# Kernel optimization log

Measured on AMD Instinct MI355X. Metric: run time of the kernel, lower is better.

Reference implementation:

```python
import jax, jax.numpy as jnp
import numpy as np


def setup_inputs() -> dict:
    key = jax.random.key(0)
    k1, k2 = jax.random.split(key)
    x = jax.random.normal(k1, (64, 32, 32, 128), dtype=jnp.float32)
    embeddings = jax.random.normal(k2, (128, 1024), dtype=jnp.float32)  # (embedding_dim, num_embeddings)
    return {"x": x, "embeddings": embeddings}


def reference(x, embeddings):
    d = embeddings.shape[0]
    flat = x.reshape(-1, d)  # [N, d]
    # squared L2 distances: ||f||^2 + ||e||^2 - 2 f.e
    similarity = flat @ embeddings  # [N, K]
    distances = (jnp.sum(flat * flat, axis=1, keepdims=True)
                 + jnp.sum(embeddings * embeddings, axis=0)
                 - 2.0 * similarity)
    idx = jnp.argmin(distances, axis=1)  # [N]
    # gather codes (equivalent to one_hot @ embeddings^T)
    quantized = embeddings.T[idx].reshape(x.shape)
    # straight-through estimator
    quantized = x + jax.lax.stop_gradient(quantized - x)
    return quantized
```

## Files before the change

### kernel.cpp

```cpp
#include <hip/hip_runtime.h>


#define NROWS 65536
#define DDIM 128
#define KCODES 1024
#define MARGIN1 0.004f

typedef __attribute__((ext_vector_type(8))) short short8;
typedef __attribute__((ext_vector_type(16))) float f32x16;

__device__ inline ushort f2bf(float f) {
    union { float f; unsigned u; } v; v.f = f;
    unsigned r = v.u + 0x7fffu + ((v.u >> 16) & 1u);
    return (ushort)(r >> 16);
}
__device__ inline float bf2f(ushort b) {
    union { unsigned u; float f; } v; v.u = ((unsigned)b) << 16;
    return v.f;
}

__device__ inline void gload_lds16(const uint4* g, uint4* lds) {
    __builtin_amdgcn_global_load_lds((const __attribute__((address_space(1))) void*)g,
                                     (__attribute__((address_space(3))) void*)lds,
                                     16, 0, 0);
}

__global__ void k_prep(const float* __restrict__ e, float* __restrict__ et,
                       float* __restrict__ nrm, double* __restrict__ nrm64,
                       uint4* __restrict__ epq) {
    const int gid = blockIdx.x * blockDim.x + threadIdx.x;

    {
        int d = gid >> 10, k = gid & 1023;
        et[k * DDIM + d] = e[gid];
    }

    if (gid < 32768) {
        int lane = gid & 63, c = (gid >> 6) & 7, h = (gid >> 9) & 1, nt = gid >> 10;
        int col = nt * 32 + (lane & 31);
        int kbase = c * 16 + ((lane >> 5) << 3);
        union { ushort u[8]; uint4 q; } pk;
        #pragma unroll
        for (int j = 0; j < 8; ++j) {
            float v = e[(kbase + j) * KCODES + col];
            ushort hb = f2bf(v);
            pk.u[j] = (h == 0) ? hb : f2bf(v - bf2f(hb));
        }
        epq[(size_t)nt * 1024 + h * 512 + c * 64 + lane] = pk.q;
    }

    if (gid >= 32768 && gid < 32768 + 8192) {
        int t2 = gid - 32768;
        int k = t2 >> 3, part = t2 & 7;
        double s = 0.0;
        #pragma unroll
        for (int j = 0; j < 16; ++j) {
            double v = (double)e[(part * 16 + j) * KCODES + k];
            s = fma(v, v, s);
        }
        #pragma unroll
        for (int m = 1; m < 8; m <<= 1) s += __shfl_xor(s, m);
        if (part == 0) { nrm64[k] = s; nrm[k] = (float)s; }
    }
}

__global__ __launch_bounds__(256, 2) void k_argmin32(const float* __restrict__ x,
                                                     const uint4* __restrict__ epq,
                                                     const float* __restrict__ nrm,
                                                     float* __restrict__ pb1,
                                                     float* __restrict__ pb2,
                                                     int* __restrict__ pbi) {
    __shared__ uint4 sbuf[2][1024];
    __shared__ float snrm[512];

    const int tid = threadIdx.x;
    const int lane = tid & 63;
    const int w = tid >> 6;
    const int kh = blockIdx.x & 1;
    const int rg = blockIdx.x >> 1;
    const int rt = rg * 4 + w;
    const int lrow = lane & 31;
    const int lgrp = lane >> 5;
    const int tbase = kh * 16;

    #pragma unroll
    for (int i = 0; i < 4; ++i)
        gload_lds16(epq + (size_t)tbase * 1024 + i * 256 + tid,
                    &sbuf[0][i * 256 + (w << 6)]);

    snrm[tid] = nrm[kh * 512 + tid];
    snrm[256 + tid] = nrm[kh * 512 + 256 + tid];

    const float* xr = x + (size_t)(rt * 32 + lrow) * DDIM + (lgrp << 3);
    short8 ah[8], al[8];
    #pragma unroll
    for (int c = 0; c < 8; ++c) {
        float4 u = *reinterpret_cast<const float4*>(xr + c * 16);
        float4 v = *reinterpret_cast<const float4*>(xr + c * 16 + 4);
        float fv[8] = {u.x, u.y, u.z, u.w, v.x, v.y, v.z, v.w};
        short8 hi, lo;
        #pragma unroll
        for (int j = 0; j < 8; ++j) {
            ushort hb = f2bf(fv[j]);
            hi[j] = (short)hb;
            lo[j] = (short)f2bf(fv[j] - bf2f(hb));
        }
        ah[c] = hi; al[c] = lo;
    }

    float b1[16], b2[16]; int bi[16];
    #pragma unroll
    for (int r = 0; r < 16; ++r) { b1[r] = 3.4e38f; b2[r] = 3.4e38f; bi[r] = 0; }

    __syncthreads();

    int cur = 0;
    for (int t = 0; t < 16; ++t) {
        if (t + 1 < 16) {
            #pragma unroll
            for (int i = 0; i < 4; ++i)
                gload_lds16(epq + (size_t)(tbase + t + 1) * 1024 + i * 256 + tid,
                            &sbuf[cur ^ 1][i * 256 + (w << 6)]);
        }
        const int lcode = t * 32 + lrow;
        const float nv = snrm[lcode];
        const int code = kh * 512 + lcode;

        f32x16 accA, accB;
        #pragma unroll
        for (int r = 0; r < 16; ++r) { accA[r] = 0.f; accB[r] = 0.f; }

        #pragma unroll
        for (int c = 0; c < 8; ++c) {
            union { uint4 q; short8 s; } bh, bl;
            bh.q = sbuf[cur][c * 64 + lane];
            bl.q = sbuf[cur][512 + c * 64 + lane];
            accA = __builtin_amdgcn_mfma_f32_32x32x16_bf16(ah[c], bh.s, accA, 0, 0, 0);
            accA = __builtin_amdgcn_mfma_f32_32x32x16_bf16(ah[c], bl.s, accA, 0, 0, 0);
            accB = __builtin_amdgcn_mfma_f32_32x32x16_bf16(al[c], bh.s, accB, 0, 0, 0);
        }

        #pragma unroll
        for (int r = 0; r < 16; ++r) {
            float s = fmaf(-2.f, accA[r] + accB[r], nv);
            b2[r] = fminf(fmaxf(s, b1[r]), b2[r]);
            bool lt = s < b1[r];
            b1[r] = lt ? s : b1[r];
            bi[r] = lt ? code : bi[r];
        }
        __syncthreads();
        cur ^= 1;
    }

    #pragma unroll
    for (int r = 0; r < 16; ++r) {
        #pragma unroll
        for (int m = 1; m < 32; m <<= 1) {
            float o1 = __shfl_xor(b1[r], m);
            float o2 = __shfl_xor(b2[r], m);
            int   oi = __shfl_xor(bi[r], m);
            bool take = (o1 < b1[r]) || (o1 == b1[r] && oi < bi[r]);
            float loser = take ? b1[r] : o1;
            b1[r] = take ? o1 : b1[r];
            bi[r] = take ? oi : bi[r];
            b2[r] = fminf(fminf(b2[r], o2), loser);
        }
    }

    if (lrow == 0) {
        #pragma unroll
        for (int r = 0; r < 16; ++r) {
            int rl = (r & 3) + 8 * (r >> 2) + 4 * lgrp;
            size_t o = (size_t)kh * NROWS + rt * 32 + rl;
            pb1[o] = b1[r]; pb2[o] = b2[r]; pbi[o] = bi[r];
        }
    }
}

__global__ void k_merge(const float* __restrict__ pb1, const float* __restrict__ pb2,
                        const int* __restrict__ pbi, int* __restrict__ idx,
                        int* __restrict__ wlc, int* __restrict__ wl) {
    int r = blockIdx.x * blockDim.x + threadIdx.x;
    float a1 = pb1[r], a2 = pb2[r];
    int   ai = pbi[r];
    float c1 = pb1[NROWS + r], c2 = pb2[NROWS + r];
    int   ci = pbi[NROWS + r];
    bool take = c1 < a1;
    float f1 = take ? c1 : a1;
    int   fi = take ? ci : ai;
    float loser = take ? a1 : c1;
    float f2 = fminf(fminf(a2, c2), loser);
    idx[r] = fi;
    if (f2 - f1 < MARGIN1) {
        int slot = atomicAdd(wlc, 1);
        wl[slot] = r;
    }
}

__global__ __launch_bounds__(256) void k_fix(const float* __restrict__ x,
                                             const float* __restrict__ e,
                                             const double* __restrict__ nrm64,
                                             const int* __restrict__ wlc,
                                             const int* __restrict__ wl,
                                             int* __restrict__ idx) {
    __shared__ float  xs[DDIM];
    __shared__ double w1[4]; __shared__ int wi[4];
    const int tid = threadIdx.x;
    const int lane = tid & 63;
    const int wv = tid >> 6;
    const int n = *wlc;

    for (int i = blockIdx.x; i < n; i += gridDim.x) {
        const int row = wl[i];
        if (tid < DDIM) xs[tid] = x[(size_t)row * DDIM + tid];
        __syncthreads();

        double dot[4] = {0.0, 0.0, 0.0, 0.0};
        for (int d0 = 0; d0 < DDIM; d0 += 8) {
            float ef[8][4];
            #pragma unroll
            for (int dd = 0; dd < 8; ++dd)
                #pragma unroll
                for (int kk = 0; kk < 4; ++kk)
                    ef[dd][kk] = e[(d0 + dd) * KCODES + tid + kk * 256];
            #pragma unroll
            for (int dd = 0; dd < 8; ++dd) {
                double xv = (double)xs[d0 + dd];
                #pragma unroll
                for (int kk = 0; kk < 4; ++kk)
                    dot[kk] = fma(xv, (double)ef[dd][kk], dot[kk]);
            }
        }

        double bb1 = 1e300; int bbi = 0;
        #pragma unroll
        for (int kk = 0; kk < 4; ++kk) {
            int k = tid + kk * 256;
            double sc = nrm64[k] - 2.0 * dot[kk];
            if (sc < bb1) { bb1 = sc; bbi = k; }
        }
        #pragma unroll
        for (int m = 1; m < 64; m <<= 1) {
            double o1 = __shfl_xor(bb1, m);
            int    oi = __shfl_xor(bbi, m);
            bool take = (o1 < bb1) || (o1 == bb1 && oi < bbi);
            bb1 = take ? o1 : bb1;
            bbi = take ? oi : bbi;
        }
        if (lane == 0) { w1[wv] = bb1; wi[wv] = bbi; }
        __syncthreads();
        if (tid == 0) {
            double f1 = w1[0]; int fi = wi[0];
            #pragma unroll
            for (int j = 1; j < 4; ++j) {
                bool take = (w1[j] < f1) || (w1[j] == f1 && wi[j] < fi);
                f1 = take ? w1[j] : f1;
                fi = take ? wi[j] : fi;
            }
            idx[row] = fi;
        }
        __syncthreads();
    }
}

__global__ void k_gather(const float* __restrict__ x, const float* __restrict__ et,
                         const int* __restrict__ idxp, float* __restrict__ out) {
    int gid = blockIdx.x * blockDim.x + threadIdx.x;
    int row = gid >> 5, d4 = gid & 31;
    float4 q = reinterpret_cast<const float4*>(et)[(size_t)idxp[row] * 32 + d4];
    float4 xv = reinterpret_cast<const float4*>(x)[gid];
    float4 o;
    o.x = xv.x + (q.x - xv.x);
    o.y = xv.y + (q.y - xv.y);
    o.z = xv.z + (q.z - xv.z);
    o.w = xv.w + (q.w - xv.w);
    reinterpret_cast<float4*>(out)[gid] = o;
}

extern "C" void kernel_launch(void* const* d_in, const int* in_sizes, int n_in,
                              void* d_out, int out_size, void* d_ws, size_t ws_size,
                              hipStream_t stream) {
    const float* x = (const float*)d_in[0];
    const float* e = (const float*)d_in[1];
    float* out = (float*)d_out;

    double* nrm64 = (double*)d_ws;
    float*  et    = (float*)d_ws + 2048;
    float*  nrm   = et + 131072;
    int*    idx   = (int*)(nrm + 1024);
    int*    wlc   = idx + NROWS;
    int*    wl    = wlc + 4;
    uint4*  epq   = (uint4*)(wl + NROWS);
    float*  pb1   = (float*)(epq + 32768);
    float*  pb2   = pb1 + 2 * NROWS;
    int*    pbi   = (int*)(pb2 + 2 * NROWS);

    hipMemsetAsync(wlc, 0, sizeof(int), stream);

    k_prep<<<512, 256, 0, stream>>>(e, et, nrm, nrm64, epq);
    k_argmin32<<<1024, 256, 0, stream>>>(x, epq, nrm, pb1, pb2, pbi);
    k_merge<<<NROWS / 256, 256, 0, stream>>>(pb1, pb2, pbi, idx, wlc, wl);
    k_fix<<<64, 256, 0, stream>>>(x, e, nrm64, wlc, wl, idx);
    k_gather<<<(NROWS * 32) / 256, 256, 0, stream>>>(x, et, idx, out);
}
```

Measured before the change: 108.6 us.

## Use single bf16 MFMA coarse argmin with packed-key tracking and rescan near-ties

The main argmin pass drops the hi/lo bf16 split, running one MFMA per chunk instead of three. It also drops LDS staging in favour of direct global loads, and tracks max-similarity keys with the tile index packed into the low mantissa bits. Rows whose top-two gap is below a wider margin go to a new rescan kernel that redoes the split-precision distance over all codes. Only rows still within the tight margin reach the fp64 fix pass. This trades much less MFMA work in the bulk pass for an extra kernel and a rescan cost that grows with how many rows fall inside the wide margin.

```diff
diff --git a/kernel.cpp b/kernel.cpp
--- a/kernel.cpp
+++ b/kernel.cpp
@@ -4,7 +4,8 @@
 #define NROWS 65536
 #define DDIM 128
 #define KCODES 1024
-#define MARGIN1 0.004f
+#define MARGIN1 0.6f
+#define MARGIN2 0.004f
 
 typedef __attribute__((ext_vector_type(8))) short short8;
 typedef __attribute__((ext_vector_type(16))) float f32x16;
@@ -17,12 +18,6 @@
 __device__ inline float bf2f(ushort b) {
     union { unsigned u; float f; } v; v.u = ((unsigned)b) << 16;
     return v.f;
-}
-
-__device__ inline void gload_lds16(const uint4* g, uint4* lds) {
-    __builtin_amdgcn_global_load_lds((const __attribute__((address_space(1))) void*)g,
-                                     (__attribute__((address_space(3))) void*)lds,
-                                     16, 0, 0);
 }
 
 __global__ void k_prep(const float* __restrict__ e, float* __restrict__ et,
@@ -70,109 +65,79 @@
                                                      float* __restrict__ pb1,
                                                      float* __restrict__ pb2,
                                                      int* __restrict__ pbi) {
-    __shared__ uint4 sbuf[2][1024];
-    __shared__ float snrm[512];
-
     const int tid = threadIdx.x;
     const int lane = tid & 63;
     const int w = tid >> 6;
     const int kh = blockIdx.x & 1;
-    const int rg = blockIdx.x >> 1;
-    const int rt = rg * 4 + w;
+    const int rt = (blockIdx.x >> 1) * 4 + w;
     const int lrow = lane & 31;
     const int lgrp = lane >> 5;
     const int tbase = kh * 16;
 
-    #pragma unroll
-    for (int i = 0; i < 4; ++i)
-        gload_lds16(epq + (size_t)tbase * 1024 + i * 256 + tid,
-                    &sbuf[0][i * 256 + (w << 6)]);
-
-    snrm[tid] = nrm[kh * 512 + tid];
-    snrm[256 + tid] = nrm[kh * 512 + 256 + tid];
-
     const float* xr = x + (size_t)(rt * 32 + lrow) * DDIM + (lgrp << 3);
-    short8 ah[8], al[8];
+    short8 ah[8];
     #pragma unroll
     for (int c = 0; c < 8; ++c) {
         float4 u = *reinterpret_cast<const float4*>(xr + c * 16);
         float4 v = *reinterpret_cast<const float4*>(xr + c * 16 + 4);
         float fv[8] = {u.x, u.y, u.z, u.w, v.x, v.y, v.z, v.w};
-        short8 hi, lo;
-        #pragma unroll
-        for (int j = 0; j < 8; ++j) {
-            ushort hb = f2bf(fv[j]);
-            hi[j] = (short)hb;
-            lo[j] = (short)f2bf(fv[j] - bf2f(hb));
-        }
-        ah[c] = hi; al[c] = lo;
-    }
-
-    float b1[16], b2[16]; int bi[16];
+        short8 hi;
+        #pragma unroll
+        for (int j = 0; j < 8; ++j) hi[j] = (short)f2bf(fv[j]);
+        ah[c] = hi;
+    }
+
+    float kb1[16], kb2[16];
     #pragma unroll
-    for (int r = 0; r < 16; ++r) { b1[r] = 3.4e38f; b2[r] = 3.4e38f; bi[r] = 0; }
-
-    __syncthreads();
-
-    int cur = 0;
+    for (int r = 0; r < 16; ++r) { kb1[r] = -3.4e38f; kb2[r] = -3.4e38f; }
+
     for (int t = 0; t < 16; ++t) {
-        if (t + 1 < 16) {
-            #pragma unroll
-            for (int i = 0; i < 4; ++i)
-                gload_lds16(epq + (size_t)(tbase + t + 1) * 1024 + i * 256 + tid,
-                            &sbuf[cur ^ 1][i * 256 + (w << 6)]);
-        }
-        const int lcode = t * 32 + lrow;
-        const float nv = snrm[lcode];
-        const int code = kh * 512 + lcode;
-
-        f32x16 accA, accB;
-        #pragma unroll
-        for (int r = 0; r < 16; ++r) { accA[r] = 0.f; accB[r] = 0.f; }
+        const int nt = tbase + t;
+        const float nv = nrm[nt * 32 + lrow];
+
+        f32x16 acc;
+        #pragma unroll
+        for (int r = 0; r < 16; ++r) acc[r] = 0.f;
 
         #pragma unroll
         for (int c = 0; c < 8; ++c) {
-            union { uint4 q; short8 s; } bh, bl;
-            bh.q = sbuf[cur][c * 64 + lane];
-            bl.q = sbuf[cur][512 + c * 64 + lane];
-            accA = __builtin_amdgcn_mfma_f32_32x32x16_bf16(ah[c], bh.s, accA, 0, 0, 0);
-            accA = __builtin_amdgcn_mfma_f32_32x32x16_bf16(ah[c], bl.s, accA, 0, 0, 0);
-            accB = __builtin_amdgcn_mfma_f32_32x32x16_bf16(al[c], bh.s, accB, 0, 0, 0);
+            union { uint4 q; short8 s; } b;
+            b.q = epq[(size_t)nt * 1024 + c * 64 + lane];
+            acc = __builtin_amdgcn_mfma_f32_32x32x16_bf16(ah[c], b.s, acc, 0, 0, 0);
         }
 
         #pragma unroll
         for (int r = 0; r < 16; ++r) {
-            float s = fmaf(-2.f, accA[r] + accB[r], nv);
-            b2[r] = fminf(fmaxf(s, b1[r]), b2[r]);
-            bool lt = s < b1[r];
-            b1[r] = lt ? s : b1[r];
-            bi[r] = lt ? code : bi[r];
-        }
-        __syncthreads();
-        cur ^= 1;
+            float m = fmaf(-0.5f, nv, acc[r]);
+            float key = __uint_as_float((__float_as_uint(m) & 0xFFFFFFF0u) | (unsigned)t);
+            kb2[r] = fmaxf(kb2[r], fminf(key, kb1[r]));
+            kb1[r] = fmaxf(kb1[r], key);
+        }
     }
 
     #pragma unroll
     for (int r = 0; r < 16; ++r) {
-        #pragma unroll
-        for (int m = 1; m < 32; m <<= 1) {
-            float o1 = __shfl_xor(b1[r], m);
-            float o2 = __shfl_xor(b2[r], m);
-            int   oi = __shfl_xor(bi[r], m);
-            bool take = (o1 < b1[r]) || (o1 == b1[r] && oi < bi[r]);
-            float loser = take ? b1[r] : o1;
-            b1[r] = take ? o1 : b1[r];
-            bi[r] = take ? oi : bi[r];
-            b2[r] = fminf(fminf(b2[r], o2), loser);
-        }
-    }
-
-    if (lrow == 0) {
-        #pragma unroll
-        for (int r = 0; r < 16; ++r) {
+        unsigned u1 = __float_as_uint(kb1[r]);
+        int code = (tbase + (int)(u1 & 15u)) * 32 + lrow;
+        float m1 = __uint_as_float(u1 & 0xFFFFFFF0u);
+        float m2 = __uint_as_float(__float_as_uint(kb2[r]) & 0xFFFFFFF0u);
+        #pragma unroll
+        for (int mm = 1; mm < 32; mm <<= 1) {
+            float o1 = __shfl_xor(m1, mm);
+            float o2 = __shfl_xor(m2, mm);
+            int   oc = __shfl_xor(code, mm);
+            bool take = (o1 > m1) || (o1 == m1 && oc < code);
+            float loser = take ? m1 : o1;
+            m1 = take ? o1 : m1;
+            code = take ? oc : code;
+            m2 = fmaxf(fmaxf(m2, o2), loser);
+        }
+        if (lrow == 0) {
             int rl = (r & 3) + 8 * (r >> 2) + 4 * lgrp;
             size_t o = (size_t)kh * NROWS + rt * 32 + rl;
-            pb1[o] = b1[r]; pb2[o] = b2[r]; pbi[o] = bi[r];
+            pb1[o] = -2.f * m1;
+            pb2[o] = -2.f * m2;
+            pbi[o] = code;
         }
     }
 }
@@ -197,6 +162,101 @@
     }
 }
 
+__global__ __launch_bounds__(256, 2) void k_rescan(const float* __restrict__ x,
+                                                   const uint4* __restrict__ epq,
+                                                   const float* __restrict__ nrm,
+                                                   const int* __restrict__ wlc,
+                                                   const int* __restrict__ wl,
+                                                   int* __restrict__ idx,
+                                                   int* __restrict__ wl2c,
+                                                   int* __restrict__ wl2) {
+    const int tid = threadIdx.x;
+    const int lane = tid & 63;
+    const int w = tid >> 6;
+    const int lrow = lane & 31;
+    const int lgrp = lane >> 5;
+    const int n = *wlc;
+    const int ntiles = (n + 31) >> 5;
+
+    for (int it = blockIdx.x * 4 + w; it < ntiles; it += gridDim.x * 4) {
+        int li = it * 32 + lrow;
+        int rowl = wl[li < n ? li : 0];
+
+        const float* xr = x + (size_t)rowl * DDIM + (lgrp << 3);
+        short8 ah[8], al[8];
+        #pragma unroll
+        for (int c = 0; c < 8; ++c) {
+            float4 u = *reinterpret_cast<const float4*>(xr + c * 16);
+            float4 v = *reinterpret_cast<const float4*>(xr + c * 16 + 4);
+            float fv[8] = {u.x, u.y, u.z, u.w, v.x, v.y, v.z, v.w};
+            short8 hi, lo;
+            #pragma unroll
+            for (int j = 0; j < 8; ++j) {
+                ushort hb = f2bf(fv[j]);
+                hi[j] = (short)hb;
+                lo[j] = (short)f2bf(fv[j] - bf2f(hb));
+            }
+            ah[c] = hi; al[c] = lo;
+        }
+
+        float b1[16], b2[16]; int bi[16];
+        #pragma unroll
+        for (int r = 0; r < 16; ++r) { b1[r] = 3.4e38f; b2[r] = 3.4e38f; bi[r] = 0; }
+
+        for (int t = 0; t < 32; ++t) {
+            const float nv = nrm[t * 32 + lrow];
+            const int code = t * 32 + lrow;
+            f32x16 accA, accB;
+            #pragma unroll
+            for (int r = 0; r < 16; ++r) { accA[r] = 0.f; accB[r] = 0.f; }
+            #pragma unroll
+            for (int c = 0; c < 8; ++c) {
+                union { uint4 q; short8 s; } bh, bl;
+                bh.q = epq[(size_t)t * 1024 + c * 64 + lane];
+                bl.q = epq[(size_t)t * 1024 + 512 + c * 64 + lane];
+                accA = __builtin_amdgcn_mfma_f32_32x32x16_bf16(ah[c], bh.s, accA, 0, 0, 0);
+                accA = __builtin_amdgcn_mfma_f32_32x32x16_bf16(ah[c], bl.s, accA, 0, 0, 0);
+                accB = __builtin_amdgcn_mfma_f32_32x32x16_bf16(al[c], bh.s, accB, 0, 0, 0);
+            }
+            #pragma unroll
+            for (int r = 0; r < 16; ++r) {
+                float s = fmaf(-2.f, accA[r] + accB[r], nv);
+                b2[r] = fminf(fmaxf(s, b1[r]), b2[r]);
+                bool lt = s < b1[r];
+                b1[r] = lt ? s : b1[r];
+                bi[r] = lt ? code : bi[r];
+            }
+        }
+
+        #pragma unroll
+        for (int r = 0; r < 16; ++r) {
+            #pragma unroll
+            for (int mm = 1; mm < 32; mm <<= 1) {
+                float o1 = __shfl_xor(b1[r], mm);
+                float o2 = __shfl_xor(b2[r], mm);
+                int   oi = __shfl_xor(bi[r], mm);
+                bool take = (o1 < b1[r]) || (o1 == b1[r] && oi < bi[r]);
+                float loser = take ? b1[r] : o1;
+                b1[r] = take ? o1 : b1[r];
+                bi[r] = take ? oi : bi[r];
+                b2[r] = fminf(fminf(b2[r], o2), loser);
+            }
+            if (lrow == 0) {
+                int rl = (r & 3) + 8 * (r >> 2) + 4 * lgrp;
+                int lj = it * 32 + rl;
+                if (lj < n) {
+                    int row = wl[lj];
+                    idx[row] = bi[r];
+                    if (b2[r] - b1[r] < MARGIN2) {
+                        int slot = atomicAdd(wl2c, 1);
+                        wl2[slot] = row;
+                    }
+                }
+            }
+        }
+    }
+}
+
 __global__ __launch_bounds__(256) void k_fix(const float* __restrict__ x,
                                              const float* __restrict__ e,
                                              const double* __restrict__ nrm64,
@@ -290,16 +350,18 @@
     int*    idx   = (int*)(nrm + 1024);
     int*    wlc   = idx + NROWS;
     int*    wl    = wlc + 4;
-    uint4*  epq   = (uint4*)(wl + NROWS);
+    int*    wl2   = wl + NROWS;
+    uint4*  epq   = (uint4*)(wl2 + NROWS);
     float*  pb1   = (float*)(epq + 32768);
     float*  pb2   = pb1 + 2 * NROWS;
     int*    pbi   = (int*)(pb2 + 2 * NROWS);
 
-    hipMemsetAsync(wlc, 0, sizeof(int), stream);
+    hipMemsetAsync(wlc, 0, 2 * sizeof(int), stream);
 
     k_prep<<<512, 256, 0, stream>>>(e, et, nrm, nrm64, epq);
     k_argmin32<<<1024, 256, 0, stream>>>(x, epq, nrm, pb1, pb2, pbi);
     k_merge<<<NROWS / 256, 256, 0, stream>>>(pb1, pb2, pbi, idx, wlc, wl);
-    k_fix<<<64, 256, 0, stream>>>(x, e, nrm64, wlc, wl, idx);
+    k_rescan<<<256, 256, 0, stream>>>(x, epq, nrm, wlc, wl, idx, wlc + 1, wl2);
+    k_fix<<<64, 256, 0, stream>>>(x, e, nrm64, wlc + 1, wl2, idx);
     k_gather<<<(NROWS * 32) / 256, 256, 0, stream>>>(x, et, idx, out);
 }
```

Result: slower. 163.0 us (+50.1%).
